# Kernel tuning notes

Hardware: AMD Instinct MI355X
Metric: run time of the kernel (lower is better)

The kernel has to match this reference:

```python
import jax, jax.numpy as jnp
import numpy as np

V, E, H, ENC, L, B, S = 32000, 512, 1024, 1024, 2, 64, 256


def setup_inputs() -> dict:
    key = jax.random.key(0)
    ks = jax.random.split(key, 20)
    sc = 0.02
    inp = {
        "input_token": jax.random.randint(ks[0], (B,), 0, V),
        "hidden": jax.random.normal(ks[1], (L, B, H), jnp.float32),
        "cell": jax.random.normal(ks[2], (L, B, H), jnp.float32),
        "encoder_outputs": jax.random.normal(ks[3], (B, S, ENC), jnp.float32),
        "mask": jax.random.randint(ks[4], (B, S), 0, 2).astype(jnp.int32),
        # parameters
        "embedding": jax.random.normal(ks[5], (V, E), jnp.float32) * sc,
        "Wq": jax.random.normal(ks[6], (H, H), jnp.float32) * sc,
        "Wk": jax.random.normal(ks[7], (H, ENC), jnp.float32) * sc,
        "v": jax.random.normal(ks[8], (H,), jnp.float32) * sc,
        "Wih0": jax.random.normal(ks[9], (4 * H, E + ENC), jnp.float32) * sc,
        "Whh0": jax.random.normal(ks[10], (4 * H, H), jnp.float32) * sc,
        "bih0": jnp.zeros((4 * H,), jnp.float32),
        "bhh0": jnp.zeros((4 * H,), jnp.float32),
        "Wih1": jax.random.normal(ks[11], (4 * H, H), jnp.float32) * sc,
        "Whh1": jax.random.normal(ks[12], (4 * H, H), jnp.float32) * sc,
        "bih1": jnp.zeros((4 * H,), jnp.float32),
        "bhh1": jnp.zeros((4 * H,), jnp.float32),
        "Wout": jax.random.normal(ks[13], (V, H + ENC + E), jnp.float32) * sc,
        "bout": jnp.zeros((V,), jnp.float32),
    }
    return inp


def _lstm_cell(x, h, c, Wih, Whh, bih, bhh):
    # PyTorch gate order: i, f, g, o
    gates = x @ Wih.T + h @ Whh.T + bih + bhh  # [B, 4H]
    i, f, g, o = jnp.split(gates, 4, axis=-1)
    c_new = jax.nn.sigmoid(f) * c + jax.nn.sigmoid(i) * jnp.tanh(g)
    h_new = jax.nn.sigmoid(o) * jnp.tanh(c_new)
    return h_new, c_new


def reference(input_token, hidden, cell, encoder_outputs, mask,
              embedding, Wq, Wk, v,
              Wih0, Whh0, bih0, bhh0, Wih1, Whh1, bih1, bhh1,
              Wout, bout):
    embedded = embedding[input_token]                      # [B, E]
    # Bahdanau additive attention (query = top-layer hidden state)
    query = hidden[-1] @ Wq.T                              # [B, H]
    keys = jnp.einsum("bse,he->bsh", encoder_outputs, Wk) # [B, S, H]
    energy = jnp.tanh(query[:, None, :] + keys) @ v       # [B, S]
    energy = jnp.where(mask == 0, -1e10, energy)
    attn_weights = jax.nn.softmax(energy, axis=1)          # [B, S]
    context = jnp.einsum("bs,bse->be", attn_weights, encoder_outputs)  # [B, ENC]
    # stacked single-step LSTM
    x0 = jnp.concatenate([embedded, context], axis=1)      # [B, E+ENC]
    h0, c0 = _lstm_cell(x0, hidden[0], cell[0], Wih0, Whh0, bih0, bhh0)
    h1, c1 = _lstm_cell(h0, hidden[1], cell[1], Wih1, Whh1, bih1, bhh1)
    new_hidden = jnp.stack([h0, h1], axis=0)
    new_cell = jnp.stack([c0, c1], axis=0)
    # output projection over concat(output, context, embedded)
    feat = jnp.concatenate([h1, context, embedded], axis=1)  # [B, H+ENC+E]
    prediction = feat @ Wout.T + bout                        # [B, V]
    return prediction, new_hidden, new_cell, attn_weights
```

## Files before the change

### kernel.cpp

```cpp
#include <hip/hip_runtime.h>
#include <hip/hip_bf16.h>

#define DEV __device__ __forceinline__

typedef __attribute__((ext_vector_type(8))) short bf16x8;
typedef __attribute__((ext_vector_type(4))) float f32x4;

static constexpr int Bsz = 64, S = 256, H = 1024, E = 512, ENCD = 1024, V = 32000;

DEV unsigned short f2bf(float f) {
    unsigned u = __builtin_bit_cast(unsigned, f);
    unsigned r = (u + 0x7FFFu + ((u >> 16) & 1u)) >> 16;
    return (unsigned short)r;
}
DEV float sigmoidf_(float x) { return 1.0f / (1.0f + __expf(-x)); }

__global__ void prep_kernel(const int* __restrict__ tok, const float* __restrict__ hidden,
                            const float* __restrict__ emb,
                            unsigned short* __restrict__ A0, unsigned short* __restrict__ A1,
                            unsigned short* __restrict__ FEAT) {
    int b = blockIdx.x, t = threadIdx.x;
    int tb = tok[b];
    for (int c = t; c < E; c += 256) {
        unsigned short us = f2bf(emb[(size_t)tb * E + c]);
        A0[b * 2560 + c] = us;
        FEAT[b * 2560 + 2048 + c] = us;
    }
    for (int c = t; c < H; c += 256) {
        A0[b * 2560 + 1536 + c] = f2bf(hidden[b * H + c]);
        A1[b * 2048 + 1024 + c] = f2bf(hidden[Bsz * H + b * H + c]);
    }
}

__global__ __launch_bounds__(256) void keys_energy_kernel(
        const float* __restrict__ enc, const float* __restrict__ Wk,
        const float* __restrict__ query, const float* __restrict__ vvec,
        float* __restrict__ energy) {
    __shared__ __align__(16) unsigned short At[128 * 40];
    __shared__ __align__(16) unsigned short Bt[128 * 40];

    int blk = blockIdx.x;
    int xcd = blk & 7, idx = blk >> 3;
    int bn = idx & 7, bml = idx >> 3;
    int bm = xcd * 16 + bml;
    int rm0 = bm * 128, n0 = bn * 128;

    int t = threadIdx.x;
    int lane = t & 63, w = t >> 6;
    int l15 = lane & 15, lg = lane >> 4;
    int r = t >> 1, seg = t & 1;
    int wrow = (w >> 1) * 64, wcol = (w & 1) * 64;

    const float* Ag = enc + (size_t)(rm0 + r) * ENCD + seg * 16;
    const float* Bg = Wk  + (size_t)(n0  + r) * ENCD + seg * 16;

    f32x4 acc[4][4];
#pragma unroll
    for (int m = 0; m < 4; ++m)
#pragma unroll
        for (int n = 0; n < 4; ++n) acc[m][n] = (f32x4)0.0f;

    for (int kk = 0; kk < 32; ++kk) {
        int k0 = kk * 32;
        float4 a0 = *(const float4*)(Ag + k0);
        float4 a1 = *(const float4*)(Ag + k0 + 4);
        float4 a2 = *(const float4*)(Ag + k0 + 8);
        float4 a3 = *(const float4*)(Ag + k0 + 12);
        float4 b0 = *(const float4*)(Bg + k0);
        float4 b1 = *(const float4*)(Bg + k0 + 4);
        float4 b2 = *(const float4*)(Bg + k0 + 8);
        float4 b3 = *(const float4*)(Bg + k0 + 12);

        bf16x8 pa0, pa1, pb0, pb1;
        pa0[0]=f2bf(a0.x); pa0[1]=f2bf(a0.y); pa0[2]=f2bf(a0.z); pa0[3]=f2bf(a0.w);
        pa0[4]=f2bf(a1.x); pa0[5]=f2bf(a1.y); pa0[6]=f2bf(a1.z); pa0[7]=f2bf(a1.w);
        pa1[0]=f2bf(a2.x); pa1[1]=f2bf(a2.y); pa1[2]=f2bf(a2.z); pa1[3]=f2bf(a2.w);
        pa1[4]=f2bf(a3.x); pa1[5]=f2bf(a3.y); pa1[6]=f2bf(a3.z); pa1[7]=f2bf(a3.w);
        pb0[0]=f2bf(b0.x); pb0[1]=f2bf(b0.y); pb0[2]=f2bf(b0.z); pb0[3]=f2bf(b0.w);
        pb0[4]=f2bf(b1.x); pb0[5]=f2bf(b1.y); pb0[6]=f2bf(b1.z); pb0[7]=f2bf(b1.w);
        pb1[0]=f2bf(b2.x); pb1[1]=f2bf(b2.y); pb1[2]=f2bf(b2.z); pb1[3]=f2bf(b2.w);
        pb1[4]=f2bf(b3.x); pb1[5]=f2bf(b3.y); pb1[6]=f2bf(b3.z); pb1[7]=f2bf(b3.w);

        __syncthreads();
        *(bf16x8*)&At[r * 40 + seg * 16]     = pa0;
        *(bf16x8*)&At[r * 40 + seg * 16 + 8] = pa1;
        *(bf16x8*)&Bt[r * 40 + seg * 16]     = pb0;
        *(bf16x8*)&Bt[r * 40 + seg * 16 + 8] = pb1;
        __syncthreads();

        bf16x8 af[4], bfv[4];
#pragma unroll
        for (int m = 0; m < 4; ++m)
            af[m] = *(const bf16x8*)&At[(wrow + m * 16 + l15) * 40 + lg * 8];
#pragma unroll
        for (int n = 0; n < 4; ++n)
            bfv[n] = *(const bf16x8*)&Bt[(wcol + n * 16 + l15) * 40 + lg * 8];
#pragma unroll
        for (int m = 0; m < 4; ++m)
#pragma unroll
            for (int n = 0; n < 4; ++n)
                acc[m][n] = __builtin_amdgcn_mfma_f32_16x16x32_bf16(af[m], bfv[n], acc[m][n], 0, 0, 0);
    }

    int b = rm0 >> 8;
    const float* qrow = query + b * H;
#pragma unroll
    for (int m = 0; m < 4; ++m) {
#pragma unroll
        for (int j = 0; j < 4; ++j) {
            int gr = rm0 + wrow + m * 16 + lg * 4 + j;
            float part = 0.f;
#pragma unroll
            for (int nf = 0; nf < 4; ++nf) {
                int gc = n0 + wcol + nf * 16 + l15;
                float val = acc[m][nf][j] + qrow[gc];
                part += vvec[gc] * tanhf(val);
            }
            part += __shfl_xor(part, 1);
            part += __shfl_xor(part, 2);
            part += __shfl_xor(part, 4);
            part += __shfl_xor(part, 8);
            if (l15 == 0) atomicAdd(&energy[gr], part);
        }
    }
}

__global__ void softmax_ctx_kernel(const float* __restrict__ energy, const int* __restrict__ mask,
                                   const float* __restrict__ enc, float* __restrict__ attn_out,
                                   unsigned short* __restrict__ A0, unsigned short* __restrict__ FEAT) {
    int b = blockIdx.x >> 2, cq = blockIdx.x & 3;
    int t = threadIdx.x;
    __shared__ float wsm[256];
    __shared__ float red[256];

    float e = energy[b * S + t];
    if (mask[b * S + t] == 0) e = -1e10f;
    red[t] = e; __syncthreads();
    for (int o = 128; o > 0; o >>= 1) { if (t < o) red[t] = fmaxf(red[t], red[t + o]); __syncthreads(); }
    float mx = red[0]; __syncthreads();
    float ex = __expf(e - mx);
    red[t] = ex; __syncthreads();
    for (int o = 128; o > 0; o >>= 1) { if (t < o) red[t] += red[t + o]; __syncthreads(); }
    float sum = red[0];
    float wt = ex / sum;
    wsm[t] = wt;
    if (cq == 0) attn_out[b * S + t] = wt;
    __syncthreads();

    int c = cq * 256 + t;
    float acc = 0.f;
    for (int s = 0; s < S; ++s) acc += wsm[s] * enc[((size_t)b * S + s) * ENCD + c];
    unsigned short us = f2bf(acc);
    A0[b * 2560 + 512 + c] = us;
    FEAT[b * 2560 + 1024 + c] = us;
}

template <int NT>
__global__ __launch_bounds__(256) void gemm_skinny_kernel(
        const unsigned short* __restrict__ A, int lda,
        const float* __restrict__ W1, int K1,
        const float* __restrict__ W2, int K2,
        const float* __restrict__ b1, const float* __restrict__ b2,
        float* __restrict__ C, int ldc) {
    constexpr int NF = NT / 16;
    __shared__ float red[4 * 64 * NT];

    int n0 = blockIdx.x * NT;
    int t = threadIdx.x, w = t >> 6, lane = t & 63;
    int l15 = lane & 15, lg = lane >> 4;
    int K = K1 + K2, Kw = K >> 2;
    int kbeg = w * Kw, kend = kbeg + Kw;

    f32x4 acc[4][NF];
#pragma unroll
    for (int m = 0; m < 4; ++m)
#pragma unroll
        for (int nf = 0; nf < NF; ++nf) acc[m][nf] = (f32x4)0.0f;

    for (int k0 = kbeg; k0 < kend; k0 += 32) {
        bf16x8 af[4];
#pragma unroll
        for (int m = 0; m < 4; ++m)
            af[m] = *(const bf16x8*)&A[(size_t)(m * 16 + l15) * lda + k0 + lg * 8];

#pragma unroll
        for (int nf = 0; nf < NF; ++nf) {
            int n = n0 + nf * 16 + l15;
            const float* base = (k0 < K1) ? (W1 + (size_t)n * K1 + k0 + lg * 8)
                                          : (W2 + (size_t)n * K2 + (k0 - K1) + lg * 8);
            float4 f0 = *(const float4*)base;
            float4 f1 = *(const float4*)(base + 4);
            bf16x8 bv;
            bv[0]=f2bf(f0.x); bv[1]=f2bf(f0.y); bv[2]=f2bf(f0.z); bv[3]=f2bf(f0.w);
            bv[4]=f2bf(f1.x); bv[5]=f2bf(f1.y); bv[6]=f2bf(f1.z); bv[7]=f2bf(f1.w);
#pragma unroll
            for (int m = 0; m < 4; ++m)
                acc[m][nf] = __builtin_amdgcn_mfma_f32_16x16x32_bf16(af[m], bv, acc[m][nf], 0, 0, 0);
        }
    }

    float* myred = red + w * 64 * NT;
#pragma unroll
    for (int m = 0; m < 4; ++m)
#pragma unroll
        for (int nf = 0; nf < NF; ++nf)
#pragma unroll
            for (int j = 0; j < 4; ++j)
                myred[(m * 16 + lg * 4 + j) * NT + nf * 16 + l15] = acc[m][nf][j];
    __syncthreads();

    for (int o = t; o < 64 * NT; o += 256) {
        int row = o / NT, col = o % NT;
        float s = red[o] + red[64 * NT + o] + red[2 * 64 * NT + o] + red[3 * 64 * NT + o];
        int n = n0 + col;
        if (b1) s += b1[n];
        if (b2) s += b2[n];
        C[(size_t)row * ldc + n] = s;
    }
}

__global__ void lstm_act_kernel(const float* __restrict__ gates, const float* __restrict__ cell_in,
                                float* __restrict__ h_out, float* __restrict__ c_out,
                                unsigned short* __restrict__ hbf, int hbf_stride) {
    int b = blockIdx.x, t = threadIdx.x;
    for (int c = t; c < H; c += 256) {
        float gi = gates[b * 4096 + c];
        float gf = gates[b * 4096 + 1024 + c];
        float gg = gates[b * 4096 + 2048 + c];
        float go = gates[b * 4096 + 3072 + c];
        float cn = sigmoidf_(gf) * cell_in[b * H + c] + sigmoidf_(gi) * tanhf(gg);
        float hn = sigmoidf_(go) * tanhf(cn);
        c_out[b * H + c] = cn;
        h_out[b * H + c] = hn;
        hbf[b * hbf_stride + c] = f2bf(hn);
    }
}

extern "C" void kernel_launch(void* const* d_in, const int* in_sizes, int n_in,
                              void* d_out, int out_size, void* d_ws, size_t ws_size,
                              hipStream_t stream) {
    const int*   tok   = (const int*)d_in[0];
    const float* hidden= (const float*)d_in[1];
    const float* cell  = (const float*)d_in[2];
    const float* enc   = (const float*)d_in[3];
    const int*   mask  = (const int*)d_in[4];
    const float* emb   = (const float*)d_in[5];
    const float* Wq    = (const float*)d_in[6];
    const float* Wk    = (const float*)d_in[7];
    const float* vvec  = (const float*)d_in[8];
    const float* Wih0  = (const float*)d_in[9];
    const float* Whh0  = (const float*)d_in[10];
    const float* bih0  = (const float*)d_in[11];
    const float* bhh0  = (const float*)d_in[12];
    const float* Wih1  = (const float*)d_in[13];
    const float* Whh1  = (const float*)d_in[14];
    const float* bih1  = (const float*)d_in[15];
    const float* bhh1  = (const float*)d_in[16];
    const float* Wout  = (const float*)d_in[17];
    const float* bout  = (const float*)d_in[18];

    float* out      = (float*)d_out;
    float* pred     = out;
    float* hid_out  = out + (size_t)Bsz * V;
    float* cell_out = hid_out + 2 * Bsz * H;
    float* attn_out = cell_out + 2 * Bsz * H;

    char* ws = (char*)d_ws;
    float* query  = (float*)ws;
    float* energy = query + Bsz * H;
    float* gates  = energy + Bsz * S;
    unsigned short* A0   = (unsigned short*)(gates + Bsz * 4096);
    unsigned short* A1   = A0 + Bsz * 2560;
    unsigned short* FEAT = A1 + Bsz * 2048;

    hipMemsetAsync(energy, 0, (size_t)Bsz * S * sizeof(float), stream);
    prep_kernel<<<Bsz, 256, 0, stream>>>(tok, hidden, emb, A0, A1, FEAT);

    gemm_skinny_kernel<16><<<H / 16, 256, 0, stream>>>(
        A1 + 1024, 2048, Wq, 1024, nullptr, 0, nullptr, nullptr, query, H);

    keys_energy_kernel<<<1024, 256, 0, stream>>>(enc, Wk, query, vvec, energy);

    softmax_ctx_kernel<<<Bsz * 4, 256, 0, stream>>>(energy, mask, enc, attn_out, A0, FEAT);

    gemm_skinny_kernel<16><<<4096 / 16, 256, 0, stream>>>(
        A0, 2560, Wih0, 1536, Whh0, 1024, bih0, bhh0, gates, 4096);
    lstm_act_kernel<<<Bsz, 256, 0, stream>>>(gates, cell, hid_out, cell_out, A1, 2048);

    gemm_skinny_kernel<16><<<4096 / 16, 256, 0, stream>>>(
        A1, 2048, Wih1, 1024, Whh1, 1024, bih1, bhh1, gates, 4096);
    lstm_act_kernel<<<Bsz, 256, 0, stream>>>(gates, cell + Bsz * H, hid_out + Bsz * H,
                                             cell_out + Bsz * H, FEAT, 2560);

    gemm_skinny_kernel<64><<<V / 64, 256, 0, stream>>>(
        FEAT, 2560, Wout, 2560, nullptr, 0, bout, nullptr, pred, V);
}
```

Before: 751.1 us.

## Pre-convert encoder outputs and Wk to bf16, add LDS-direct loads and new output GEMM

Adds a pass that converts encoder_outputs and Wk to bf16 in workspace once per call. The keys/energy GEMM then streams bf16 through global_load_lds into XOR-swizzled shared tiles with a 64-wide K step, and softmax/context reads the bf16 copy using wave-shuffle reductions with one block per batch row. The output projection switches from the split-K skinny GEMM to a per-wave GEMM that streams Wout with register prefetch and needs no LDS reduction. The conversion adds an extra full read and write of the 64 MB encoder tensor. Context accumulation also now uses bf16-rounded encoder values.

```diff
diff --git a/kernel.cpp b/kernel.cpp
--- a/kernel.cpp
+++ b/kernel.cpp
@@ -13,7 +13,28 @@
     unsigned r = (u + 0x7FFFu + ((u >> 16) & 1u)) >> 16;
     return (unsigned short)r;
 }
+DEV float bf2f(unsigned short us) {
+    return __builtin_bit_cast(float, (unsigned)us << 16);
+}
 DEV float sigmoidf_(float x) { return 1.0f / (1.0f + __expf(-x)); }
+
+DEV void gload_lds16(const unsigned short* g, unsigned short* l) {
+    __builtin_amdgcn_global_load_lds(
+        (const __attribute__((address_space(1))) unsigned int*)g,
+        (__attribute__((address_space(3))) unsigned int*)l, 16, 0, 0);
+}
+
+__global__ void convert_bf16_kernel(const float* __restrict__ src,
+                                    unsigned short* __restrict__ dst, int n8) {
+    int i = blockIdx.x * blockDim.x + threadIdx.x;
+    if (i >= n8) return;
+    float4 f0 = ((const float4*)src)[(size_t)i * 2];
+    float4 f1 = ((const float4*)src)[(size_t)i * 2 + 1];
+    bf16x8 v;
+    v[0]=f2bf(f0.x); v[1]=f2bf(f0.y); v[2]=f2bf(f0.z); v[3]=f2bf(f0.w);
+    v[4]=f2bf(f1.x); v[5]=f2bf(f1.y); v[6]=f2bf(f1.z); v[7]=f2bf(f1.w);
+    ((bf16x8*)dst)[i] = v;
+}
 
 __global__ void prep_kernel(const int* __restrict__ tok, const float* __restrict__ hidden,
                             const float* __restrict__ emb,
@@ -33,11 +54,11 @@
 }
 
 __global__ __launch_bounds__(256) void keys_energy_kernel(
-        const float* __restrict__ enc, const float* __restrict__ Wk,
+        const unsigned short* __restrict__ encb, const unsigned short* __restrict__ Wkb,
         const float* __restrict__ query, const float* __restrict__ vvec,
         float* __restrict__ energy) {
-    __shared__ __align__(16) unsigned short At[128 * 40];
-    __shared__ __align__(16) unsigned short Bt[128 * 40];
+    __shared__ __align__(16) unsigned short At[128 * 64];
+    __shared__ __align__(16) unsigned short Bt[128 * 64];
 
     int blk = blockIdx.x;
     int xcd = blk & 7, idx = blk >> 3;
@@ -48,58 +69,51 @@
     int t = threadIdx.x;
     int lane = t & 63, w = t >> 6;
     int l15 = lane & 15, lg = lane >> 4;
-    int r = t >> 1, seg = t & 1;
     int wrow = (w >> 1) * 64, wcol = (w & 1) * 64;
 
-    const float* Ag = enc + (size_t)(rm0 + r) * ENCD + seg * 16;
-    const float* Bg = Wk  + (size_t)(n0  + r) * ENCD + seg * 16;
-
     f32x4 acc[4][4];
 #pragma unroll
     for (int m = 0; m < 4; ++m)
 #pragma unroll
         for (int n = 0; n < 4; ++n) acc[m][n] = (f32x4)0.0f;
 
-    for (int kk = 0; kk < 32; ++kk) {
-        int k0 = kk * 32;
-        float4 a0 = *(const float4*)(Ag + k0);
-        float4 a1 = *(const float4*)(Ag + k0 + 4);
-        float4 a2 = *(const float4*)(Ag + k0 + 8);
-        float4 a3 = *(const float4*)(Ag + k0 + 12);
-        float4 b0 = *(const float4*)(Bg + k0);
-        float4 b1 = *(const float4*)(Bg + k0 + 4);
-        float4 b2 = *(const float4*)(Bg + k0 + 8);
-        float4 b3 = *(const float4*)(Bg + k0 + 12);
-
-        bf16x8 pa0, pa1, pb0, pb1;
-        pa0[0]=f2bf(a0.x); pa0[1]=f2bf(a0.y); pa0[2]=f2bf(a0.z); pa0[3]=f2bf(a0.w);
-        pa0[4]=f2bf(a1.x); pa0[5]=f2bf(a1.y); pa0[6]=f2bf(a1.z); pa0[7]=f2bf(a1.w);
-        pa1[0]=f2bf(a2.x); pa1[1]=f2bf(a2.y); pa1[2]=f2bf(a2.z); pa1[3]=f2bf(a2.w);
-        pa1[4]=f2bf(a3.x); pa1[5]=f2bf(a3.y); pa1[6]=f2bf(a3.z); pa1[7]=f2bf(a3.w);
-        pb0[0]=f2bf(b0.x); pb0[1]=f2bf(b0.y); pb0[2]=f2bf(b0.z); pb0[3]=f2bf(b0.w);
-        pb0[4]=f2bf(b1.x); pb0[5]=f2bf(b1.y); pb0[6]=f2bf(b1.z); pb0[7]=f2bf(b1.w);
-        pb1[0]=f2bf(b2.x); pb1[1]=f2bf(b2.y); pb1[2]=f2bf(b2.z); pb1[3]=f2bf(b2.w);
-        pb1[4]=f2bf(b3.x); pb1[5]=f2bf(b3.y); pb1[6]=f2bf(b3.z); pb1[7]=f2bf(b3.w);
-
+    int srow = lane >> 3;
+    int scol_xor = lane & 7;
+
+    for (int kk = 0; kk < 16; ++kk) {
+        int k0 = kk * 64;
         __syncthreads();
-        *(bf16x8*)&At[r * 40 + seg * 16]     = pa0;
-        *(bf16x8*)&At[r * 40 + seg * 16 + 8] = pa1;
-        *(bf16x8*)&Bt[r * 40 + seg * 16]     = pb0;
-        *(bf16x8*)&Bt[r * 40 + seg * 16 + 8] = pb1;
+#pragma unroll
+        for (int i = 0; i < 4; ++i) {
+            int c = w * 4 + i;
+            int row = c * 8 + srow;
+            int sc = ((scol_xor ^ (row & 7)) * 8);
+            gload_lds16(encb + (size_t)(rm0 + row) * ENCD + k0 + sc, &At[c * 512]);
+            gload_lds16(Wkb  + (size_t)(n0  + row) * ENCD + k0 + sc, &Bt[c * 512]);
+        }
         __syncthreads();
 
-        bf16x8 af[4], bfv[4];
-#pragma unroll
-        for (int m = 0; m < 4; ++m)
-            af[m] = *(const bf16x8*)&At[(wrow + m * 16 + l15) * 40 + lg * 8];
-#pragma unroll
-        for (int n = 0; n < 4; ++n)
-            bfv[n] = *(const bf16x8*)&Bt[(wcol + n * 16 + l15) * 40 + lg * 8];
-#pragma unroll
-        for (int m = 0; m < 4; ++m)
-#pragma unroll
-            for (int n = 0; n < 4; ++n)
-                acc[m][n] = __builtin_amdgcn_mfma_f32_16x16x32_bf16(af[m], bfv[n], acc[m][n], 0, 0, 0);
+#pragma unroll
+        for (int ks = 0; ks < 2; ++ks) {
+            bf16x8 af[4], bfv[4];
+#pragma unroll
+            for (int m = 0; m < 4; ++m) {
+                int row = wrow + m * 16 + l15;
+                int off = row * 128 + ((ks * 64 + lg * 16) ^ ((row & 7) << 4));
+                af[m] = *(const bf16x8*)((const char*)At + off);
+            }
+#pragma unroll
+            for (int n = 0; n < 4; ++n) {
+                int row = wcol + n * 16 + l15;
+                int off = row * 128 + ((ks * 64 + lg * 16) ^ ((row & 7) << 4));
+                bfv[n] = *(const bf16x8*)((const char*)Bt + off);
+            }
+#pragma unroll
+            for (int m = 0; m < 4; ++m)
+#pragma unroll
+                for (int n = 0; n < 4; ++n)
+                    acc[m][n] = __builtin_amdgcn_mfma_f32_16x16x32_bf16(af[m], bfv[n], acc[m][n], 0, 0, 0);
+        }
     }
 
     int b = rm0 >> 8;
@@ -125,34 +139,49 @@
     }
 }
 
-__global__ void softmax_ctx_kernel(const float* __restrict__ energy, const int* __restrict__ mask,
-                                   const float* __restrict__ enc, float* __restrict__ attn_out,
-                                   unsigned short* __restrict__ A0, unsigned short* __restrict__ FEAT) {
-    int b = blockIdx.x >> 2, cq = blockIdx.x & 3;
-    int t = threadIdx.x;
+__global__ __launch_bounds__(256) void softmax_ctx_kernel(
+        const float* __restrict__ energy, const int* __restrict__ mask,
+        const unsigned short* __restrict__ encb, float* __restrict__ attn_out,
+        unsigned short* __restrict__ A0, unsigned short* __restrict__ FEAT) {
+    int b = blockIdx.x, t = threadIdx.x;
     __shared__ float wsm[256];
-    __shared__ float red[256];
+    __shared__ float red[8];
 
     float e = energy[b * S + t];
     if (mask[b * S + t] == 0) e = -1e10f;
-    red[t] = e; __syncthreads();
-    for (int o = 128; o > 0; o >>= 1) { if (t < o) red[t] = fmaxf(red[t], red[t + o]); __syncthreads(); }
-    float mx = red[0]; __syncthreads();
+    float m = e;
+#pragma unroll
+    for (int o = 32; o > 0; o >>= 1) m = fmaxf(m, __shfl_xor(m, o));
+    if ((t & 63) == 0) red[t >> 6] = m;
+    __syncthreads();
+    float mx = fmaxf(fmaxf(red[0], red[1]), fmaxf(red[2], red[3]));
     float ex = __expf(e - mx);
-    red[t] = ex; __syncthreads();
-    for (int o = 128; o > 0; o >>= 1) { if (t < o) red[t] += red[t + o]; __syncthreads(); }
-    float sum = red[0];
+    float sm = ex;
+#pragma unroll
+    for (int o = 32; o > 0; o >>= 1) sm += __shfl_xor(sm, o);
+    if ((t & 63) == 0) red[4 + (t >> 6)] = sm;
+    __syncthreads();
+    float sum = red[4] + red[5] + red[6] + red[7];
     float wt = ex / sum;
     wsm[t] = wt;
-    if (cq == 0) attn_out[b * S + t] = wt;
+    attn_out[b * S + t] = wt;
     __syncthreads();
 
-    int c = cq * 256 + t;
-    float acc = 0.f;
-    for (int s = 0; s < S; ++s) acc += wsm[s] * enc[((size_t)b * S + s) * ENCD + c];
-    unsigned short us = f2bf(acc);
-    A0[b * 2560 + 512 + c] = us;
-    FEAT[b * 2560 + 1024 + c] = us;
+    int c = t * 4;
+    float a0 = 0.f, a1 = 0.f, a2 = 0.f, a3 = 0.f;
+    const unsigned short* ep = encb + (size_t)b * S * ENCD + c;
+#pragma unroll 4
+    for (int s2 = 0; s2 < S; ++s2) {
+        float w_ = wsm[s2];
+        ushort4 u = *(const ushort4*)(ep + (size_t)s2 * ENCD);
+        a0 += w_ * bf2f(u.x); a1 += w_ * bf2f(u.y);
+        a2 += w_ * bf2f(u.z); a3 += w_ * bf2f(u.w);
+    }
+    unsigned short o0 = f2bf(a0), o1 = f2bf(a1), o2 = f2bf(a2), o3 = f2bf(a3);
+    A0[b * 2560 + 512 + c] = o0;  A0[b * 2560 + 512 + c + 1] = o1;
+    A0[b * 2560 + 512 + c + 2] = o2; A0[b * 2560 + 512 + c + 3] = o3;
+    FEAT[b * 2560 + 1024 + c] = o0; FEAT[b * 2560 + 1024 + c + 1] = o1;
+    FEAT[b * 2560 + 1024 + c + 2] = o2; FEAT[b * 2560 + 1024 + c + 3] = o3;
 }
 
 template <int NT>
@@ -217,6 +246,48 @@
         if (b2) s += b2[n];
         C[(size_t)row * ldc + n] = s;
     }
+}
+
+__global__ __launch_bounds__(256) void gemm_wide_kernel(
+        const unsigned short* __restrict__ A, int lda, int K,
+        const float* __restrict__ W, const float* __restrict__ bias,
+        float* __restrict__ C, int ldc) {
+    int t = threadIdx.x, w = t >> 6, lane = t & 63;
+    int l15 = lane & 15, lg = lane >> 4;
+    int n = blockIdx.x * 64 + w * 16 + l15;
+
+    const float* wp = W + (size_t)n * K + lg * 8;
+    f32x4 acc[4];
+#pragma unroll
+    for (int m = 0; m < 4; ++m) acc[m] = (f32x4)0.0f;
+
+    float4 c0 = *(const float4*)(wp);
+    float4 c1 = *(const float4*)(wp + 4);
+    for (int k0 = 0; k0 < K; k0 += 32) {
+        float4 n0_ = c0, n1_ = c1;
+        if (k0 + 32 < K) {
+            n0_ = *(const float4*)(wp + 32);
+            n1_ = *(const float4*)(wp + 36);
+        }
+        bf16x8 bv;
+        bv[0]=f2bf(c0.x); bv[1]=f2bf(c0.y); bv[2]=f2bf(c0.z); bv[3]=f2bf(c0.w);
+        bv[4]=f2bf(c1.x); bv[5]=f2bf(c1.y); bv[6]=f2bf(c1.z); bv[7]=f2bf(c1.w);
+        bf16x8 af[4];
+#pragma unroll
+        for (int m = 0; m < 4; ++m)
+            af[m] = *(const bf16x8*)&A[(size_t)(m * 16 + l15) * lda + k0 + lg * 8];
+#pragma unroll
+        for (int m = 0; m < 4; ++m)
+            acc[m] = __builtin_amdgcn_mfma_f32_16x16x32_bf16(af[m], bv, acc[m], 0, 0, 0);
+        c0 = n0_; c1 = n1_; wp += 32;
+    }
+
+    float bs = bias ? bias[n] : 0.f;
+#pragma unroll
+    for (int m = 0; m < 4; ++m)
+#pragma unroll
+        for (int j = 0; j < 4; ++j)
+            C[(size_t)(m * 16 + lg * 4 + j) * ldc + n] = acc[m][j] + bs;
 }
 
 __global__ void lstm_act_kernel(const float* __restrict__ gates, const float* __restrict__ cell_in,
@@ -272,16 +343,20 @@
     unsigned short* A0   = (unsigned short*)(gates + Bsz * 4096);
     unsigned short* A1   = A0 + Bsz * 2560;
     unsigned short* FEAT = A1 + Bsz * 2048;
-
+    unsigned short* encb = FEAT + Bsz * 2560;
+    unsigned short* Wkb  = encb + (size_t)Bsz * S * ENCD;
+
+    convert_bf16_kernel<<<(Bsz * S * ENCD / 8) / 256, 256, 0, stream>>>(enc, encb, Bsz * S * ENCD / 8);
+    convert_bf16_kernel<<<(H * ENCD / 8) / 256, 256, 0, stream>>>(Wk, Wkb, H * ENCD / 8);
     hipMemsetAsync(energy, 0, (size_t)Bsz * S * sizeof(float), stream);
     prep_kernel<<<Bsz, 256, 0, stream>>>(tok, hidden, emb, A0, A1, FEAT);
 
     gemm_skinny_kernel<16><<<H / 16, 256, 0, stream>>>(
         A1 + 1024, 2048, Wq, 1024, nullptr, 0, nullptr, nullptr, query, H);
 
-    keys_energy_kernel<<<1024, 256, 0, stream>>>(enc, Wk, query, vvec, energy);
-
-    softmax_ctx_kernel<<<Bsz * 4, 256, 0, stream>>>(energy, mask, enc, attn_out, A0, FEAT);
+    keys_energy_kernel<<<1024, 256, 0, stream>>>(encb, Wkb, query, vvec, energy);
+
+    softmax_ctx_kernel<<<Bsz, 256, 0, stream>>>(energy, mask, encb, attn_out, A0, FEAT);
 
     gemm_skinny_kernel<16><<<4096 / 16, 256, 0, stream>>>(
         A0, 2560, Wih0, 1536, Whh0, 1024, bih0, bhh0, gates, 4096);
@@ -292,6 +367,6 @@
     lstm_act_kernel<<<Bsz, 256, 0, stream>>>(gates, cell + Bsz * H, hid_out + Bsz * H,
                                              cell_out + Bsz * H, FEAT, 2560);
 
-    gemm_skinny_kernel<64><<<V / 64, 256, 0, stream>>>(
-        FEAT, 2560, Wout, 2560, nullptr, 0, bout, nullptr, pred, V);
-}
+    gemm_wide_kernel<<<V / 64, 256, 0, stream>>>(
+        FEAT, 2560, 2560, Wout, bout, pred, V);
+}
```

Result: no change. 761.3 us (+1.4%).
